# Optimization experiments

Measured on AMD Instinct MI355X. Metric: run time of the kernel, lower is better.

Reference implementation:

```python
import jax, jax.numpy as jnp
import numpy as np

WS = 8      # window_size
SS = 4      # shift_size
NH = 16     # num_heads


def _rel_position_index(ws):
    # matches WindowMSA.double_step_seq + flip(1)
    seq1 = np.arange(0, (2 * ws - 1) * ws, 2 * ws - 1)
    seq2 = np.arange(0, ws)
    rel = (seq1[:, None] + seq2[None, :]).reshape(1, -1)  # (1, ws*ws)
    idx = rel + rel.T                                      # (ws*ws, ws*ws)
    return np.ascontiguousarray(idx[:, ::-1]).astype(np.int32)


def _shift_attn_mask(H, W, ws, ss):
    # static numpy construction of the Swin shift mask, (nW, N, N)
    img = np.zeros((H, W), dtype=np.int32)
    slices = (slice(0, -ws), slice(-ws, -ss), slice(-ss, None))
    cnt = 0
    for h in slices:
        for w in slices:
            img[h, w] = cnt
            cnt += 1
    win = img.reshape(H // ws, ws, W // ws, ws).transpose(0, 2, 1, 3).reshape(-1, ws * ws)
    diff = win[:, None, :] - win[:, :, None]
    return np.where(diff != 0, -100.0, 0.0).astype(np.float32)


def setup_inputs() -> dict:
    key = jax.random.key(0)
    ks = jax.random.split(key, 6)
    B, H, W, C = 16, 64, 64, 512
    return {
        "query": jax.random.normal(ks[0], (B, H * W, C), jnp.float32),
        "qkv_w": jax.random.normal(ks[1], (3 * C, C), jnp.float32) * 0.02,
        "qkv_b": jnp.zeros((3 * C,), jnp.float32),
        "proj_w": jax.random.normal(ks[2], (C, C), jnp.float32) * 0.02,
        "proj_b": jnp.zeros((C,), jnp.float32),
        "bias_table": jax.random.normal(ks[3], ((2 * WS - 1) ** 2, NH), jnp.float32) * 0.02,
        "rel_index": jnp.asarray(_rel_position_index(WS)),
        "H": H,
        "W": W,
    }


def reference(query, qkv_w, qkv_b, proj_w, proj_b, bias_table, rel_index, H, W):
    B, L, C = query.shape
    hd = C // NH
    scale = hd ** -0.5
    N = WS * WS
    nW = (H // WS) * (W // WS)

    x = query.reshape(B, H, W, C)
    # cyclic shift
    x = jnp.roll(x, (-SS, -SS), axis=(1, 2))
    # window partition -> (B*nW, N, C)
    xw = x.reshape(B, H // WS, WS, W // WS, WS, C).transpose(0, 1, 3, 2, 4, 5)
    xw = xw.reshape(B * nW, N, C)

    # qkv projection
    qkv = xw @ qkv_w.T + qkv_b                       # (BnW, N, 3C)
    qkv = qkv.reshape(B * nW, N, 3, NH, hd).transpose(2, 0, 3, 1, 4)
    q, k, v = qkv[0], qkv[1], qkv[2]                 # (BnW, NH, N, hd)

    attn = jnp.einsum('whnd,whmd->whnm', q * scale, k)

    # relative position bias (N, N, NH) -> (NH, N, N)
    bias = bias_table[rel_index.reshape(-1)].reshape(N, N, NH).transpose(2, 0, 1)
    attn = attn + bias[None]

    # shift mask (static)
    mask = jnp.asarray(_shift_attn_mask(H, W, WS, SS))  # (nW, N, N)
    attn = attn.reshape(B, nW, NH, N, N) + mask[None, :, None]
    attn = jax.nn.softmax(attn.reshape(B * nW, NH, N, N), axis=-1)

    out = jnp.einsum('whnm,whmd->whnd', attn, v)     # (BnW, NH, N, hd)
    out = out.transpose(0, 2, 1, 3).reshape(B * nW, N, C)
    out = out @ proj_w.T + proj_b

    # window reverse -> (B, H, W, C)
    out = out.reshape(B, H // WS, W // WS, WS, WS, C).transpose(0, 1, 3, 2, 4, 5)
    out = out.reshape(B, H, W, C)
    # reverse cyclic shift
    out = jnp.roll(out, (SS, SS), axis=(1, 2))
    return out.reshape(B, H * W, C)
```

## Files before the change

kernel.cpp:

```cpp
#include <hip/hip_runtime.h>


typedef short  short8  __attribute__((ext_vector_type(8)));
typedef short  short4v __attribute__((ext_vector_type(4)));
typedef float  floatx4 __attribute__((ext_vector_type(4)));

#define DEVI static __device__ __forceinline__

DEVI unsigned short f2bf(float f) {
    union { float f; unsigned int u; } v;
    v.f = f;
    return (unsigned short)((v.u + 0x7fffu + ((v.u >> 16) & 1u)) >> 16);
}

__global__ void wcvt(const float* __restrict__ qkv_w,
                     const float* __restrict__ proj_w,
                     unsigned short* __restrict__ wbf) {
    const int idx = ((blockIdx.x << 8) + threadIdx.x) << 2;
    const float* src = (idx < 786432) ? (qkv_w + idx) : (proj_w + (idx - 786432));
    const floatx4 v = *(const floatx4*)src;
    short4v o;
    o[0] = (short)f2bf(v[0]); o[1] = (short)f2bf(v[1]);
    o[2] = (short)f2bf(v[2]); o[3] = (short)f2bf(v[3]);
    *(short4v*)(wbf + idx) = o;
}

__global__ void xcvt(const float* __restrict__ query,
                     unsigned short* __restrict__ xw) {
    const int bid = blockIdx.x;
    const int x   = bid & 7;
    const int s   = bid >> 3;
    const int win = (x << 7) + (s >> 4);
    const int rem = ((s & 15) << 8) + threadIdx.x;
    const int jc  = rem & 3;
    const int tok = (rem >> 2) & 63;
    const int kc  = rem >> 8;
    const int b   = win >> 6, wy = (win >> 3) & 7, wx = win & 7;
    const int ty  = tok >> 3, tx = tok & 7;
    const int gh  = ((wy << 3) + ty + 4) & 63;
    const int gw  = ((wx << 3) + tx + 4) & 63;
    const float* src = query + (((b << 12) + (gh << 6) + gw) << 9) + (kc << 5) + (jc << 3);
    const floatx4 v0 = *(const floatx4*)src;
    const floatx4 v1 = *(const floatx4*)(src + 4);
    short8 sv;
    sv[0] = (short)f2bf(v0[0]); sv[1] = (short)f2bf(v0[1]);
    sv[2] = (short)f2bf(v0[2]); sv[3] = (short)f2bf(v0[3]);
    sv[4] = (short)f2bf(v1[0]); sv[5] = (short)f2bf(v1[1]);
    sv[6] = (short)f2bf(v1[2]); sv[7] = (short)f2bf(v1[3]);
    *(short8*)(xw + (win << 15) + (kc << 11) + (tok << 5) + (jc << 3)) = sv;
}

__global__ __launch_bounds__(256, 2)
void k_fused3(const unsigned short* __restrict__ wbf,
              const unsigned short* __restrict__ xw,
              const float* __restrict__ qkv_b,
              const float* __restrict__ proj_b,
              const float* __restrict__ bias_table,
              float* __restrict__ out)
{
    __shared__ __align__(16) unsigned short smem[24576];

    const int tid  = threadIdx.x;
    const int lane = tid & 63;
    const int l15  = lane & 15;
    const int quad = lane >> 4;
    const int wave = tid >> 6;

    const int win = blockIdx.x;
    const int b   = win >> 6;
    const int wy  = (win >> 3) & 7;
    const int wx  = win & 7;
    const int mid = ((wy == 7) ? 2 : 0) | ((wx == 7) ? 1 : 0);

    unsigned short* wbs = smem + wave * 6144;
    unsigned short* qbf = wbs;
    unsigned short* kbf = wbs + 2048;
    unsigned short* vT  = wbs + 4096;
    unsigned short* pbf = wbs;

    const int sw4 = (l15 & 3) ^ (l15 >> 2);
    const int sw8 = (l15 & 7) ^ (l15 >> 3);

    const unsigned short* xa = xw + (win << 15) + (l15 << 5) + (quad << 3);
    const float scale = 0.17677669529663687f;
    const floatx4 fz = {0.f, 0.f, 0.f, 0.f};

    unsigned int po[4][16];

    for (int hh = 0; hh < 4; ++hh) {
        const int h = (wave << 2) + hh;

        floatx4 accq[4][2], acck[4][2], accv[4][2];
        #pragma unroll
        for (int mt = 0; mt < 4; ++mt)
            #pragma unroll
            for (int nt = 0; nt < 2; ++nt) { accq[mt][nt] = fz; acck[mt][nt] = fz; accv[mt][nt] = fz; }

        const unsigned short* wq = wbf + ((h << 5) + l15) * 512 + (quad << 3);
        const unsigned short* wk = wq + 262144;
        const unsigned short* wv = wk + 262144;

        #pragma unroll 2
        for (int kk = 0; kk < 512; kk += 32) {
            short8 a[4], bq[2], bk2[2], bv2[2];
            #pragma unroll
            for (int mt = 0; mt < 4; ++mt)
                a[mt] = *(const short8*)(xa + (kk << 6) + (mt << 9));
            #pragma unroll
            for (int nt = 0; nt < 2; ++nt) {
                const int ro = (nt << 4) * 512 + kk;
                bq[nt]  = *(const short8*)(wq + ro);
                bk2[nt] = *(const short8*)(wk + ro);
                bv2[nt] = *(const short8*)(wv + ro);
            }
            #pragma unroll
            for (int nt = 0; nt < 2; ++nt)
                #pragma unroll
                for (int mt = 0; mt < 4; ++mt) {
                    accq[mt][nt] = __builtin_amdgcn_mfma_f32_16x16x32_bf16(a[mt], bq[nt],  accq[mt][nt], 0, 0, 0);
                    acck[mt][nt] = __builtin_amdgcn_mfma_f32_16x16x32_bf16(a[mt], bk2[nt], acck[mt][nt], 0, 0, 0);
                    accv[mt][nt] = __builtin_amdgcn_mfma_f32_16x16x32_bf16(a[mt], bv2[nt], accv[mt][nt], 0, 0, 0);
                }
        }

        #pragma unroll
        for (int nt = 0; nt < 2; ++nt) {
            const int cix = (h << 5) + (nt << 4) + l15;
            const float bq_ = qkv_b[cix];
            const float bk_ = qkv_b[512 + cix];
            const float bv_ = qkv_b[1024 + cix];
            #pragma unroll
            for (int mt = 0; mt < 4; ++mt) {
                short4v vv;
                #pragma unroll
                for (int r = 0; r < 4; ++r) {
                    const int row = (mt << 4) + (quad << 2) + r;
                    const int ph  = (2 * nt + (l15 >> 3)) ^ (row & 3) ^ ((row >> 2) & 3);
                    const int off = (row << 5) + (l15 & 7) + (ph << 3);
                    qbf[off] = f2bf(accq[mt][nt][r] + bq_);
                    kbf[off] = f2bf(acck[mt][nt][r] + bk_);
                    vv[r] = (short)f2bf(accv[mt][nt][r] + bv_);
                }
                const int vph = (2 * mt + (quad >> 1)) ^ sw8;
                *(short4v*)&vT[(((nt << 4) + l15) << 6) + ((quad & 1) << 2) + (vph << 3)] = vv;
            }
        }

        short8 qa[4], ka[4];
        #pragma unroll
        for (int t = 0; t < 4; ++t) {
            const int off = ((((t << 4) + l15)) << 5) + ((quad ^ sw4) << 3);
            qa[t] = *(const short8*)&qbf[off];
            ka[t] = *(const short8*)&kbf[off];
        }
        floatx4 s4[4][4];
        #pragma unroll
        for (int mt = 0; mt < 4; ++mt)
            #pragma unroll
            for (int nt = 0; nt < 4; ++nt)
                s4[mt][nt] = __builtin_amdgcn_mfma_f32_16x16x32_bf16(qa[mt], ka[nt], fz, 0, 0, 0);

        int  gjv[4]; bool jrow[4], jcol[4];
        #pragma unroll
        for (int nt = 0; nt < 4; ++nt) {
            const int j  = (nt << 4) + l15;
            const int j2 = 63 - j;
            gjv[nt]  = 15 * (j2 >> 3) + (j2 & 7);
            jrow[nt] = (j >> 3) < 4;
            jcol[nt] = (j & 7) < 4;
        }
        #pragma unroll
        for (int mt = 0; mt < 4; ++mt) {
            const int i0  = (mt << 4) + (quad << 2);
            const int fi0 = 15 * (i0 >> 3) + (i0 & 7);
            const bool irow = (i0 >> 3) < 4;
            const bool icol = (i0 & 7) == 0;
            #pragma unroll
            for (int nt = 0; nt < 4; ++nt) {
                float mval = 0.0f;
                if ((mid & 2) && (irow != jrow[nt])) mval = -100.0f;
                if ((mid & 1) && (icol != jcol[nt])) mval = -100.0f;
                const float* bp = bias_table + (fi0 + gjv[nt]) * 16 + h;
                #pragma unroll
                for (int r = 0; r < 4; ++r)
                    s4[mt][nt][r] = s4[mt][nt][r] * scale + bp[r * 16] + mval;
            }
        }

        #pragma unroll
        for (int mt = 0; mt < 4; ++mt)
            #pragma unroll
            for (int r = 0; r < 4; ++r) {
                float m = fmaxf(fmaxf(s4[mt][0][r], s4[mt][1][r]),
                                fmaxf(s4[mt][2][r], s4[mt][3][r]));
                m = fmaxf(m, __shfl_xor(m, 1));
                m = fmaxf(m, __shfl_xor(m, 2));
                m = fmaxf(m, __shfl_xor(m, 4));
                m = fmaxf(m, __shfl_xor(m, 8));
                float loc = 0.0f;
                #pragma unroll
                for (int nt = 0; nt < 4; ++nt) {
                    s4[mt][nt][r] = __expf(s4[mt][nt][r] - m);
                    loc += s4[mt][nt][r];
                }
                loc += __shfl_xor(loc, 1);
                loc += __shfl_xor(loc, 2);
                loc += __shfl_xor(loc, 4);
                loc += __shfl_xor(loc, 8);
                const float inv = 1.0f / loc;
                const int row = (mt << 4) + (quad << 2) + r;
                #pragma unroll
                for (int nt = 0; nt < 4; ++nt) {
                    const int ph = (2 * nt + (l15 >> 3)) ^ (row & 7) ^ ((row >> 3) & 1);
                    pbf[(row << 6) + (l15 & 7) + (ph << 3)] = f2bf(s4[mt][nt][r] * inv);
                }
            }

        short8 pa[4][2], va[2][2];
        #pragma unroll
        for (int mt = 0; mt < 4; ++mt)
            #pragma unroll
            for (int ks = 0; ks < 2; ++ks)
                pa[mt][ks] = *(const short8*)&pbf[((((mt << 4) + l15)) << 6) + ((((ks << 2) + quad) ^ sw8) << 3)];
        #pragma unroll
        for (int nt = 0; nt < 2; ++nt)
            #pragma unroll
            for (int ks = 0; ks < 2; ++ks)
                va[nt][ks] = *(const short8*)&vT[((((nt << 4) + l15)) << 6) + ((((ks << 2) + quad) ^ sw8) << 3)];

        #pragma unroll
        for (int mt = 0; mt < 4; ++mt)
            #pragma unroll
            for (int nt = 0; nt < 2; ++nt) {
                floatx4 acc = fz;
                acc = __builtin_amdgcn_mfma_f32_16x16x32_bf16(pa[mt][0], va[nt][0], acc, 0, 0, 0);
                acc = __builtin_amdgcn_mfma_f32_16x16x32_bf16(pa[mt][1], va[nt][1], acc, 0, 0, 0);
                const int pi = ((mt << 1) + nt) << 1;
                po[hh][pi]     = (unsigned int)f2bf(acc[0]) | ((unsigned int)f2bf(acc[1]) << 16);
                po[hh][pi + 1] = (unsigned int)f2bf(acc[2]) | ((unsigned int)f2bf(acc[3]) << 16);
            }
    }

    unsigned short* xsh = smem;
    const unsigned short* pwb = wbf + 786432;

    for (int pass = 0; pass < 2; ++pass) {
        const int co0 = (wave << 7) + (pass << 6);
        floatx4 acc[4][4];
        #pragma unroll
        for (int mt = 0; mt < 4; ++mt)
            #pragma unroll
            for (int nt = 0; nt < 4; ++nt) acc[mt][nt] = fz;

        const unsigned short* wp = pwb + (co0 + l15) * 512;

        for (int rnd = 0; rnd < 2; ++rnd) {
            __syncthreads();
            #pragma unroll
            for (int hi = 0; hi < 2; ++hi) {
                const int hh = (rnd << 1) + hi;
                const int c0 = (wave << 6) + (hi << 5) + l15;
                #pragma unroll
                for (int mt = 0; mt < 4; ++mt)
                    #pragma unroll
                    for (int nt = 0; nt < 2; ++nt) {
                        const int pi = ((mt << 1) + nt) << 1;
                        #pragma unroll
                        for (int r = 0; r < 4; ++r) {
                            const int row = (mt << 4) + (quad << 2) + r;
                            const unsigned int w = po[hh][pi + (r >> 1)];
                            xsh[row * 264 + c0 + (nt << 4)] =
                                (unsigned short)((w >> ((r & 1) << 4)) & 0xffffu);
                        }
                    }
            }
            __syncthreads();

            #pragma unroll 2
            for (int kk = 0; kk < 256; kk += 32) {
                const int rb = ((kk >> 6) << 7) + (rnd << 6) + (kk & 63) + (quad << 3);
                short8 a[4], bfr[4];
                #pragma unroll
                for (int mt = 0; mt < 4; ++mt)
                    a[mt] = *(const short8*)&xsh[((mt << 4) + l15) * 264 + kk + (quad << 3)];
                #pragma unroll
                for (int nt = 0; nt < 4; ++nt)
                    bfr[nt] = *(const short8*)(wp + (nt << 4) * 512 + rb);
                #pragma unroll
                for (int nt = 0; nt < 4; ++nt)
                    #pragma unroll
                    for (int mt = 0; mt < 4; ++mt)
                        acc[mt][nt] = __builtin_amdgcn_mfma_f32_16x16x32_bf16(a[mt], bfr[nt], acc[mt][nt], 0, 0, 0);
            }
        }

        #pragma unroll
        for (int nt = 0; nt < 4; ++nt) {
            const float pb_ = proj_b[co0 + (nt << 4) + l15];
            #pragma unroll
            for (int mt = 0; mt < 4; ++mt)
                #pragma unroll
                for (int r = 0; r < 4; ++r) {
                    const int tok = (mt << 4) + (quad << 2) + r;
                    const int ty = tok >> 3, tx = tok & 7;
                    const int gh = ((wy << 3) + ty + 4) & 63;
                    const int gw = ((wx << 3) + tx + 4) & 63;
                    out[(((b << 12) + (gh << 6) + gw) << 9) + co0 + (nt << 4) + l15] =
                        acc[mt][nt][r] + pb_;
                }
        }
    }
}

__global__ __launch_bounds__(256, 1)
void k_legacy(const float* __restrict__ query,
              const unsigned short* __restrict__ wbf,
              const float* __restrict__ qkv_b,
              const float* __restrict__ proj_b,
              const float* __restrict__ bias_table,
              float* __restrict__ out)
{
    __shared__ __align__(16) unsigned short smem[62976];

    const int tid  = threadIdx.x;
    const int lane = tid & 63;
    const int l15  = lane & 15;
    const int quad = lane >> 4;
    const int wave = tid >> 6;

    const int win = blockIdx.x;
    const int b   = win >> 6;
    const int wy  = (win >> 3) & 7;
    const int wx  = win & 7;
    const int mid = ((wy == 7) ? 2 : 0) | ((wx == 7) ? 1 : 0);

    unsigned short* xs  = smem;
    unsigned short* wb  = smem + 33280 + wave * 7424;
    unsigned short* qbf = wb;
    unsigned short* kbf = wb + 2560;
    unsigned short* vT  = wb + 5120;
    unsigned short* pbf = wb;

    #pragma unroll
    for (int it = 0; it < 32; ++it) {
        const int c   = tid + (it << 8);
        const int tok = c >> 7;
        const int fo  = (c & 127) << 2;
        const int ty  = tok >> 3, tx = tok & 7;
        const int gh  = ((wy << 3) + ty + 4) & 63;
        const int gw  = ((wx << 3) + tx + 4) & 63;
        const floatx4 v = *(const floatx4*)(query + (((b << 12) + (gh << 6) + gw) << 9) + fo);
        short4v s;
        s[0] = (short)f2bf(v[0]); s[1] = (short)f2bf(v[1]);
        s[2] = (short)f2bf(v[2]); s[3] = (short)f2bf(v[3]);
        *(short4v*)&xs[tok * 520 + fo] = s;
    }
    __syncthreads();

    const float scale = 0.17677669529663687f;
    const floatx4 fz = {0.f, 0.f, 0.f, 0.f};
    unsigned int po[4][16];

    for (int hh = 0; hh < 4; ++hh) {
        const int h = (wave << 2) + hh;
        floatx4 accq[4][2], acck[4][2], accv[4][2];
        #pragma unroll
        for (int mt = 0; mt < 4; ++mt)
            #pragma unroll
            for (int nt = 0; nt < 2; ++nt) { accq[mt][nt] = fz; acck[mt][nt] = fz; accv[mt][nt] = fz; }

        const unsigned short* wq = wbf + ((h << 5) + l15) * 512 + (quad << 3);
        const unsigned short* wk = wq + 262144;
        const unsigned short* wv = wk + 262144;

        #pragma unroll 2
        for (int kk = 0; kk < 512; kk += 32) {
            short8 a[4], bq[2], bk2[2], bv2[2];
            #pragma unroll
            for (int mt = 0; mt < 4; ++mt)
                a[mt] = *(const short8*)&xs[((mt << 4) + l15) * 520 + kk + (quad << 3)];
            #pragma unroll
            for (int nt = 0; nt < 2; ++nt) {
                const int ro = (nt << 4) * 512 + kk;
                bq[nt]  = *(const short8*)(wq + ro);
                bk2[nt] = *(const short8*)(wk + ro);
                bv2[nt] = *(const short8*)(wv + ro);
            }
            #pragma unroll
            for (int nt = 0; nt < 2; ++nt)
                #pragma unroll
                for (int mt = 0; mt < 4; ++mt) {
                    accq[mt][nt] = __builtin_amdgcn_mfma_f32_16x16x32_bf16(a[mt], bq[nt],  accq[mt][nt], 0, 0, 0);
                    acck[mt][nt] = __builtin_amdgcn_mfma_f32_16x16x32_bf16(a[mt], bk2[nt], acck[mt][nt], 0, 0, 0);
                    accv[mt][nt] = __builtin_amdgcn_mfma_f32_16x16x32_bf16(a[mt], bv2[nt], accv[mt][nt], 0, 0, 0);
                }
        }

        #pragma unroll
        for (int nt = 0; nt < 2; ++nt) {
            const int cix = (h << 5) + (nt << 4) + l15;
            const float bq_ = qkv_b[cix];
            const float bk_ = qkv_b[512 + cix];
            const float bv_ = qkv_b[1024 + cix];
            #pragma unroll
            for (int mt = 0; mt < 4; ++mt) {
                short4v vv;
                #pragma unroll
                for (int r = 0; r < 4; ++r) {
                    const int row = (mt << 4) + (quad << 2) + r;
                    qbf[row * 40 + (nt << 4) + l15] = f2bf(accq[mt][nt][r] + bq_);
                    kbf[row * 40 + (nt << 4) + l15] = f2bf(acck[mt][nt][r] + bk_);
                    vv[r] = (short)f2bf(accv[mt][nt][r] + bv_);
                }
                *(short4v*)&vT[((nt << 4) + l15) * 72 + (mt << 4) + (quad << 2)] = vv;
            }
        }

        short8 qa[4], ka[4];
        #pragma unroll
        for (int t = 0; t < 4; ++t) {
            qa[t] = *(const short8*)&qbf[((t << 4) + l15) * 40 + (quad << 3)];
            ka[t] = *(const short8*)&kbf[((t << 4) + l15) * 40 + (quad << 3)];
        }
        floatx4 s4[4][4];
        #pragma unroll
        for (int mt = 0; mt < 4; ++mt)
            #pragma unroll
            for (int nt = 0; nt < 4; ++nt)
                s4[mt][nt] = __builtin_amdgcn_mfma_f32_16x16x32_bf16(qa[mt], ka[nt], fz, 0, 0, 0);

        int  gjv[4]; bool jrow[4], jcol[4];
        #pragma unroll
        for (int nt = 0; nt < 4; ++nt) {
            const int j  = (nt << 4) + l15;
            const int j2 = 63 - j;
            gjv[nt]  = 15 * (j2 >> 3) + (j2 & 7);
            jrow[nt] = (j >> 3) < 4;
            jcol[nt] = (j & 7) < 4;
        }
        #pragma unroll
        for (int mt = 0; mt < 4; ++mt) {
            const int i0  = (mt << 4) + (quad << 2);
            const int fi0 = 15 * (i0 >> 3) + (i0 & 7);
            const bool irow = (i0 >> 3) < 4;
            const bool icol = (i0 & 7) == 0;
            #pragma unroll
            for (int nt = 0; nt < 4; ++nt) {
                float mval = 0.0f;
                if ((mid & 2) && (irow != jrow[nt])) mval = -100.0f;
                if ((mid & 1) && (icol != jcol[nt])) mval = -100.0f;
                const float* bp = bias_table + (fi0 + gjv[nt]) * 16 + h;
                #pragma unroll
                for (int r = 0; r < 4; ++r)
                    s4[mt][nt][r] = s4[mt][nt][r] * scale + bp[r * 16] + mval;
            }
        }

        #pragma unroll
        for (int mt = 0; mt < 4; ++mt)
            #pragma unroll
            for (int r = 0; r < 4; ++r) {
                float m = fmaxf(fmaxf(s4[mt][0][r], s4[mt][1][r]),
                                fmaxf(s4[mt][2][r], s4[mt][3][r]));
                m = fmaxf(m, __shfl_xor(m, 1));
                m = fmaxf(m, __shfl_xor(m, 2));
                m = fmaxf(m, __shfl_xor(m, 4));
                m = fmaxf(m, __shfl_xor(m, 8));
                float loc = 0.0f;
                #pragma unroll
                for (int nt = 0; nt < 4; ++nt) {
                    s4[mt][nt][r] = __expf(s4[mt][nt][r] - m);
                    loc += s4[mt][nt][r];
                }
                loc += __shfl_xor(loc, 1);
                loc += __shfl_xor(loc, 2);
                loc += __shfl_xor(loc, 4);
                loc += __shfl_xor(loc, 8);
                const float inv = 1.0f / loc;
                const int row = (mt << 4) + (quad << 2) + r;
                #pragma unroll
                for (int nt = 0; nt < 4; ++nt)
                    pbf[row * 72 + (nt << 4) + l15] = f2bf(s4[mt][nt][r] * inv);
            }

        short8 pa[4][2], va[2][2];
        #pragma unroll
        for (int mt = 0; mt < 4; ++mt)
            #pragma unroll
            for (int ks = 0; ks < 2; ++ks)
                pa[mt][ks] = *(const short8*)&pbf[((mt << 4) + l15) * 72 + (ks << 5) + (quad << 3)];
        #pragma unroll
        for (int nt = 0; nt < 2; ++nt)
            #pragma unroll
            for (int ks = 0; ks < 2; ++ks)
                va[nt][ks] = *(const short8*)&vT[((nt << 4) + l15) * 72 + (ks << 5) + (quad << 3)];

        #pragma unroll
        for (int mt = 0; mt < 4; ++mt)
            #pragma unroll
            for (int nt = 0; nt < 2; ++nt) {
                floatx4 acc = fz;
                acc = __builtin_amdgcn_mfma_f32_16x16x32_bf16(pa[mt][0], va[nt][0], acc, 0, 0, 0);
                acc = __builtin_amdgcn_mfma_f32_16x16x32_bf16(pa[mt][1], va[nt][1], acc, 0, 0, 0);
                const int pi = ((mt << 1) + nt) << 1;
                po[hh][pi]     = (unsigned int)f2bf(acc[0]) | ((unsigned int)f2bf(acc[1]) << 16);
                po[hh][pi + 1] = (unsigned int)f2bf(acc[2]) | ((unsigned int)f2bf(acc[3]) << 16);
            }
    }
    __syncthreads();

    #pragma unroll
    for (int hh = 0; hh < 4; ++hh) {
        const int ch0 = (((wave << 2) + hh) << 5) + l15;
        #pragma unroll
        for (int mt = 0; mt < 4; ++mt)
            #pragma unroll
            for (int nt = 0; nt < 2; ++nt) {
                const int pi = ((mt << 1) + nt) << 1;
                #pragma unroll
                for (int r = 0; r < 4; ++r) {
                    const int row = (mt << 4) + (quad << 2) + r;
                    const unsigned int w = po[hh][pi + (r >> 1)];
                    xs[row * 520 + ch0 + (nt << 4)] =
                        (unsigned short)((w >> ((r & 1) << 4)) & 0xffffu);
                }
            }
    }
    __syncthreads();

    const unsigned short* pwb = wbf + 786432;
    for (int pass = 0; pass < 2; ++pass) {
        const int co0 = (wave << 7) + (pass << 6);
        floatx4 acc[4][4];
        #pragma unroll
        for (int mt = 0; mt < 4; ++mt)
            #pragma unroll
            for (int nt = 0; nt < 4; ++nt) acc[mt][nt] = fz;

        const unsigned short* wp = pwb + (co0 + l15) * 512 + (quad << 3);

        #pragma unroll 2
        for (int kk = 0; kk < 512; kk += 32) {
            short8 a[4], bfr[4];
            #pragma unroll
            for (int mt = 0; mt < 4; ++mt)
                a[mt] = *(const short8*)&xs[((mt << 4) + l15) * 520 + kk + (quad << 3)];
            #pragma unroll
            for (int nt = 0; nt < 4; ++nt)
                bfr[nt] = *(const short8*)(wp + (nt << 4) * 512 + kk);
            #pragma unroll
            for (int nt = 0; nt < 4; ++nt)
                #pragma unroll
                for (int mt = 0; mt < 4; ++mt)
                    acc[mt][nt] = __builtin_amdgcn_mfma_f32_16x16x32_bf16(a[mt], bfr[nt], acc[mt][nt], 0, 0, 0);
        }

        #pragma unroll
        for (int nt = 0; nt < 4; ++nt) {
            const float pb_ = proj_b[co0 + (nt << 4) + l15];
            #pragma unroll
            for (int mt = 0; mt < 4; ++mt)
                #pragma unroll
                for (int r = 0; r < 4; ++r) {
                    const int tok = (mt << 4) + (quad << 2) + r;
                    const int ty = tok >> 3, tx = tok & 7;
                    const int gh = ((wy << 3) + ty + 4) & 63;
                    const int gw = ((wx << 3) + tx + 4) & 63;
                    out[(((b << 12) + (gh << 6) + gw) << 9) + co0 + (nt << 4) + l15] =
                        acc[mt][nt][r] + pb_;
                }
        }
    }
}

extern "C" void kernel_launch(void* const* d_in, const int* in_sizes, int n_in,
                              void* d_out, int out_size, void* d_ws, size_t ws_size,
                              hipStream_t stream) {
    const float* query      = (const float*)d_in[0];
    const float* qkv_w      = (const float*)d_in[1];
    const float* qkv_b      = (const float*)d_in[2];
    const float* proj_w     = (const float*)d_in[3];
    const float* proj_b     = (const float*)d_in[4];
    const float* bias_table = (const float*)d_in[5];

    unsigned short* wbf = (unsigned short*)d_ws;
    unsigned short* xw  = wbf + 1048576;

    const size_t needB = (size_t)(1048576 + 33554432) * sizeof(unsigned short);

    if (ws_size >= needB) {
        hipLaunchKernelGGL(wcvt,     dim3(1024),  dim3(256), 0, stream, qkv_w, proj_w, wbf);
        hipLaunchKernelGGL(xcvt,     dim3(16384), dim3(256), 0, stream, query, xw);
        hipLaunchKernelGGL(k_fused3, dim3(1024),  dim3(256), 0, stream,
                           wbf, xw, qkv_b, proj_b, bias_table, (float*)d_out);
    } else {
        hipLaunchKernelGGL(wcvt,     dim3(1024), dim3(256), 0, stream, qkv_w, proj_w, wbf);
        hipLaunchKernelGGL(k_legacy, dim3(1024), dim3(256), 0, stream,
                           query, wbf, qkv_b, proj_b, bias_table, (float*)d_out);
    }
}
```

Measured before the change: 482.7 us.

## Stage QKV GEMM operands in shared memory with register prefetch across waves

The QKV projection loop now loads the window activation tile and the weight rows for four heads cooperatively into shared memory once per k-step. A register prefetch of the next k-slice overlaps the global loads with the MFMA work. Head assignment is changed from four consecutive heads per wave to interleaved heads, so all waves share the same activation tile. Previously each wave loaded these from global memory redundantly. This adds two barriers per k-step, and the proj-stage channel ordering is remapped to match.

```diff
diff --git a/kernel.cpp b/kernel.cpp
--- a/kernel.cpp
+++ b/kernel.cpp
@@ -51,7 +51,7 @@
 }
 
 __global__ __launch_bounds__(256, 2)
-void k_fused3(const unsigned short* __restrict__ wbf,
+void k_fused4(const unsigned short* __restrict__ wbf,
               const unsigned short* __restrict__ xw,
               const float* __restrict__ qkv_b,
               const float* __restrict__ proj_b,
@@ -72,6 +72,8 @@
     const int wx  = win & 7;
     const int mid = ((wy == 7) ? 2 : 0) | ((wx == 7) ? 1 : 0);
 
+    unsigned short* stA = smem;
+    unsigned short* stB = smem + 2048;
     unsigned short* wbs = smem + wave * 6144;
     unsigned short* qbf = wbs;
     unsigned short* kbf = wbs + 2048;
@@ -81,14 +83,29 @@
     const int sw4 = (l15 & 3) ^ (l15 >> 2);
     const int sw8 = (l15 & 7) ^ (l15 >> 3);
 
-    const unsigned short* xa = xw + (win << 15) + (l15 << 5) + (quad << 3);
     const float scale = 0.17677669529663687f;
     const floatx4 fz = {0.f, 0.f, 0.f, 0.f};
 
     unsigned int po[4][16];
 
-    for (int hh = 0; hh < 4; ++hh) {
-        const int h = (wave << 2) + hh;
+    const int s_tok = tid >> 2;
+    const int a_ko  = (((tid & 3) ^ (s_tok & 3) ^ ((s_tok >> 2) & 3)) << 3);
+    const unsigned short* a_src = xw + (win << 15) + s_tok * 32 + a_ko;
+    const int sB    = ((tid >> 2) & 3) ^ ((tid >> 4) & 3);
+    const int b_ko  = (((tid & 3) ^ sB) << 3);
+
+    for (int hq = 0; hq < 4; ++hq) {
+        const int h = (hq << 2) + wave;
+
+        int rowb[6];
+        #pragma unroll
+        for (int i = 0; i < 6; ++i) {
+            const int cpp = (i << 6) + (tid >> 2);
+            const int mat = cpp >> 7;
+            const int wv_ = (cpp >> 5) & 3;
+            const int c   = cpp & 31;
+            rowb[i] = mat * 262144 + (((hq << 2) + wv_) * 32 + c) * 512 + b_ko;
+        }
 
         floatx4 accq[4][2], acck[4][2], accv[4][2];
         #pragma unroll
@@ -96,31 +113,44 @@
             #pragma unroll
             for (int nt = 0; nt < 2; ++nt) { accq[mt][nt] = fz; acck[mt][nt] = fz; accv[mt][nt] = fz; }
 
-        const unsigned short* wq = wbf + ((h << 5) + l15) * 512 + (quad << 3);
-        const unsigned short* wk = wq + 262144;
-        const unsigned short* wv = wk + 262144;
-
-        #pragma unroll 2
-        for (int kk = 0; kk < 512; kk += 32) {
-            short8 a[4], bq[2], bk2[2], bv2[2];
+        short8 pga, pgb[6];
+        pga = *(const short8*)a_src;
+        #pragma unroll
+        for (int i = 0; i < 6; ++i)
+            pgb[i] = *(const short8*)(wbf + rowb[i]);
+
+        for (int ks = 0; ks < 16; ++ks) {
+            const int kn = ((ks + 1) & 15) << 5;
+            *(short8*)(stA + (tid << 3)) = pga;
+            #pragma unroll
+            for (int i = 0; i < 6; ++i)
+                *(short8*)(stB + (i << 11) + (tid << 3)) = pgb[i];
+            __syncthreads();
+            pga = *(const short8*)(a_src + ((kn >> 5) << 11));
+            #pragma unroll
+            for (int i = 0; i < 6; ++i)
+                pgb[i] = *(const short8*)(wbf + rowb[i] + kn);
+            short8 af[4], bqf[2], bkf[2], bvf[2];
+            const int coff = (quad ^ sw4) << 3;
             #pragma unroll
             for (int mt = 0; mt < 4; ++mt)
-                a[mt] = *(const short8*)(xa + (kk << 6) + (mt << 9));
+                af[mt] = *(const short8*)(stA + (((mt << 4) + l15) << 5) + coff);
             #pragma unroll
             for (int nt = 0; nt < 2; ++nt) {
-                const int ro = (nt << 4) * 512 + kk;
-                bq[nt]  = *(const short8*)(wq + ro);
-                bk2[nt] = *(const short8*)(wk + ro);
-                bv2[nt] = *(const short8*)(wv + ro);
+                const int cq_ = (wave << 5) + (nt << 4) + l15;
+                bqf[nt] = *(const short8*)(stB + (cq_ << 5) + coff);
+                bkf[nt] = *(const short8*)(stB + ((128 + cq_) << 5) + coff);
+                bvf[nt] = *(const short8*)(stB + ((256 + cq_) << 5) + coff);
             }
             #pragma unroll
             for (int nt = 0; nt < 2; ++nt)
                 #pragma unroll
                 for (int mt = 0; mt < 4; ++mt) {
-                    accq[mt][nt] = __builtin_amdgcn_mfma_f32_16x16x32_bf16(a[mt], bq[nt],  accq[mt][nt], 0, 0, 0);
-                    acck[mt][nt] = __builtin_amdgcn_mfma_f32_16x16x32_bf16(a[mt], bk2[nt], acck[mt][nt], 0, 0, 0);
-                    accv[mt][nt] = __builtin_amdgcn_mfma_f32_16x16x32_bf16(a[mt], bv2[nt], accv[mt][nt], 0, 0, 0);
-                }
+                    accq[mt][nt] = __builtin_amdgcn_mfma_f32_16x16x32_bf16(af[mt], bqf[nt], accq[mt][nt], 0, 0, 0);
+                    acck[mt][nt] = __builtin_amdgcn_mfma_f32_16x16x32_bf16(af[mt], bkf[nt], acck[mt][nt], 0, 0, 0);
+                    accv[mt][nt] = __builtin_amdgcn_mfma_f32_16x16x32_bf16(af[mt], bvf[nt], accv[mt][nt], 0, 0, 0);
+                }
+            __syncthreads();
         }
 
         #pragma unroll
@@ -236,9 +266,11 @@
                 acc = __builtin_amdgcn_mfma_f32_16x16x32_bf16(pa[mt][0], va[nt][0], acc, 0, 0, 0);
                 acc = __builtin_amdgcn_mfma_f32_16x16x32_bf16(pa[mt][1], va[nt][1], acc, 0, 0, 0);
                 const int pi = ((mt << 1) + nt) << 1;
-                po[hh][pi]     = (unsigned int)f2bf(acc[0]) | ((unsigned int)f2bf(acc[1]) << 16);
-                po[hh][pi + 1] = (unsigned int)f2bf(acc[2]) | ((unsigned int)f2bf(acc[3]) << 16);
-            }
+                po[hq][pi]     = (unsigned int)f2bf(acc[0]) | ((unsigned int)f2bf(acc[1]) << 16);
+                po[hq][pi + 1] = (unsigned int)f2bf(acc[2]) | ((unsigned int)f2bf(acc[3]) << 16);
+            }
+
+        __syncthreads();
     }
 
     unsigned short* xsh = smem;
@@ -257,9 +289,9 @@
         for (int rnd = 0; rnd < 2; ++rnd) {
             __syncthreads();
             #pragma unroll
-            for (int hi = 0; hi < 2; ++hi) {
-                const int hh = (rnd << 1) + hi;
-                const int c0 = (wave << 6) + (hi << 5) + l15;
+            for (int g = 0; g < 2; ++g) {
+                const int hq = (rnd << 1) + g;
+                const int c0 = (g << 7) + (wave << 5) + l15;
                 #pragma unroll
                 for (int mt = 0; mt < 4; ++mt)
                     #pragma unroll
@@ -268,7 +300,7 @@
                         #pragma unroll
                         for (int r = 0; r < 4; ++r) {
                             const int row = (mt << 4) + (quad << 2) + r;
-                            const unsigned int w = po[hh][pi + (r >> 1)];
+                            const unsigned int w = po[hq][pi + (r >> 1)];
                             xsh[row * 264 + c0 + (nt << 4)] =
                                 (unsigned short)((w >> ((r & 1) << 4)) & 0xffffu);
                         }
@@ -278,7 +310,7 @@
 
             #pragma unroll 2
             for (int kk = 0; kk < 256; kk += 32) {
-                const int rb = ((kk >> 6) << 7) + (rnd << 6) + (kk & 63) + (quad << 3);
+                const int rb = (rnd << 8) + kk + (quad << 3);
                 short8 a[4], bfr[4];
                 #pragma unroll
                 for (int mt = 0; mt < 4; ++mt)
@@ -591,7 +623,7 @@
     if (ws_size >= needB) {
         hipLaunchKernelGGL(wcvt,     dim3(1024),  dim3(256), 0, stream, qkv_w, proj_w, wbf);
         hipLaunchKernelGGL(xcvt,     dim3(16384), dim3(256), 0, stream, query, xw);
-        hipLaunchKernelGGL(k_fused3, dim3(1024),  dim3(256), 0, stream,
+        hipLaunchKernelGGL(k_fused4, dim3(1024),  dim3(256), 0, stream,
                            wbf, xw, qkv_b, proj_b, bias_table, (float*)d_out);
     } else {
         hipLaunchKernelGGL(wcvt,     dim3(1024), dim3(256), 0, stream, qkv_w, proj_w, wbf);
```

Result: faster. 465.7 us (-3.5%).
